# Kernel optimization log

Measured on AMD Instinct MI355X. Metric: run time of the kernel, lower is better.

The kernel has to match this reference:

```python
import math
import jax, jax.numpy as jnp
import numpy as np

GRAIN = 300   # bilinear / grain dim (gpconv output channels)
PAD = 4       # explicit zero padding before each conv1d / conv2d
POOL = 40     # adaptive pool target (mf_model_pool_dim)

def conv1d_k2(x, w, b):
    # x: [B, L, Cin], w: [Cout, Cin, 2] -> [B, L-1, Cout]
    return (jnp.einsum('blc,oc->blo', x[:, :-1], w[:, :, 0])
            + jnp.einsum('blc,oc->blo', x[:, 1:], w[:, :, 1]) + b)

def kmax_last(x, k):
    # torch-style k-max pooling: top-k values along last axis, original order kept
    idx = jnp.sort(jax.lax.top_k(x, k)[1], axis=-1)
    return jnp.take_along_axis(x, idx, axis=-1)

def kmax_len(x, k):
    # k-max pooling over the length axis (axis=1) of [B, L, C]
    return jnp.swapaxes(kmax_last(jnp.swapaxes(x, 1, 2), k), 1, 2)

def adaptive_max_1d(x, out, axis):
    # torch AdaptiveMaxPool semantics along one axis; windows precomputed statically
    L = x.shape[axis]
    r = np.arange(out)
    starts = (r * L) // out
    ends = -((-(r + 1) * L) // out)
    maxw = int((ends - starts).max())
    off = starts[:, None] + np.arange(maxw)[None, :]
    mask = jnp.asarray(off < ends[:, None])
    idxs = np.minimum(off, L - 1)
    xm = jnp.moveaxis(x, axis, -1)
    g = jnp.where(mask, xm[..., idxs], -jnp.inf)
    return jnp.moveaxis(g.max(-1), -1, axis)

def conv2d_p4(x, w, b):
    y = jax.lax.conv_general_dilated(x, w, (1, 1), [(PAD, PAD), (PAD, PAD)],
                                     dimension_numbers=('NCHW', 'OIHW', 'NCHW'))
    return y + b[None, :, None, None]

def gp_tower(x, w1, b1, w2, b2, w3, b3, k1, k2):
    # multigranular conv tower: zero-pad(4) -> conv1d(k=2) -> tanh -> k-max pool
    g0 = kmax_last(x, GRAIN)                      # [B, L, 300]
    def block(z, w, b, k):
        z = jnp.pad(z, ((0, 0), (PAD, PAD), (0, 0)))
        return kmax_len(jnp.tanh(conv1d_k2(z, w, b)), k)
    p1 = block(x, w1, b1, k1)                     # [B, k1, 300]
    p2 = block(p1, w2, b2, k2)                    # [B, k2, 300]
    p3 = block(p2, w3, b3, 1)                     # [B, 1, 300]
    return jnp.concatenate([g0, p1, p2, p3], axis=1)

def _forward(query, pos_doc, neg_docs, qw1, qb1, qw2, qb2, qw3, qb3,
             dw1, db1, dw2, db2, dw3, db3, bw, bb,
             mw1, mb1, mw2, mb2, mw3, mb3, lw, lb):
    B, Lq, _ = query.shape
    S, _, Ld, _ = neg_docs.shape
    kq1, kq2 = max(4, math.ceil(2 * Lq / 3)), max(4, math.ceil(Lq / 3))
    kd1, kd2 = max(4, math.ceil(2 * Ld / 3)), max(4, math.ceil(Ld / 3))
    qg = gp_tower(query, qw1, qb1, qw2, qb2, qw3, qb3, kq1, kq2)   # [B, Nq, 300]
    docs = jnp.concatenate([pos_doc[None], neg_docs], 0).reshape((S + 1) * B, Ld, -1)
    dg = gp_tower(docs, dw1, db1, dw2, db2, dw3, db3, kd1, kd2)    # [(S+1)B, Nd, 300]
    Nq, Nd = qg.shape[1], dg.shape[1]
    dg = dg.reshape(S + 1, B, Nd, GRAIN)
    # batched bilinear matching + sigmoid (replaces the O(Nq*Nd) per-pair loop)
    qt = jnp.einsum('bqd,de->bqe', qg, bw)
    M = jax.nn.sigmoid(jnp.einsum('bqe,sbje->sbqj', qt, dg) + bb[0])
    M = M.reshape((S + 1) * B, Nq, Nd)
    x = adaptive_max_1d(adaptive_max_1d(M, POOL, 1), POOL, 2)[:, None]  # [N,1,40,40]
    for w, b in ((mw1, mb1), (mw2, mb2), (mw3, mb3)):
        x = jax.nn.sigmoid(conv2d_p4(x, w, b))
        x = adaptive_max_1d(adaptive_max_1d(x, POOL, 2), POOL, 3)
        x = x.max(axis=1, keepdims=True)          # k-max(k=1) over channels
    feat = x[:, 0]                                # [N, 40, 40]
    h = jax.nn.sigmoid(jnp.einsum('nij,j->ni', feat, lw[0]) + lb[0])
    s = jax.nn.sigmoid(h @ lw[0] + lb[0])
    return s.reshape(S + 1, B)                    # row 0 = pos-doc scores

def setup_inputs():
    ks = jax.random.split(jax.random.key(0), 26)
    def n(i, shape, s=0.05):
        return jax.random.normal(ks[i], shape, dtype=jnp.float32) * s
    return dict(
        query=jax.random.normal(ks[0], (16, 239, 1024), dtype=jnp.float32),
        pos_doc=jax.random.normal(ks[1], (16, 479, 1024), dtype=jnp.float32),
        neg_docs=jax.random.normal(ks[2], (4, 16, 479, 1024), dtype=jnp.float32),
        qw1=n(3, (300, 1024, 2)), qb1=n(4, (300,)),
        qw2=n(5, (300, 300, 2)), qb2=n(6, (300,)),
        qw3=n(7, (300, 300, 2)), qb3=n(8, (300,)),
        dw1=n(9, (300, 1024, 2)), db1=n(10, (300,)),
        dw2=n(11, (300, 300, 2)), db2=n(12, (300,)),
        dw3=n(13, (300, 300, 2)), db3=n(14, (300,)),
        bw=n(15, (300, 300)), bb=n(16, (1,)),
        mw1=n(17, (50, 1, 2, 2)), mb1=n(18, (50,)),
        mw2=n(19, (50, 1, 2, 2)), mb2=n(20, (50,)),
        mw3=n(21, (50, 1, 2, 2)), mb3=n(22, (50,)),
        lw=n(23, (1, 40)), lb=n(24, (1,)),
    )

def reference(query, pos_doc, neg_docs, qw1, qb1, qw2, qb2, qw3, qb3,
              dw1, db1, dw2, db2, dw3, db3, bw, bb,
              mw1, mb1, mw2, mb2, mw3, mb3, lw, lb):
    return _forward(query, pos_doc, neg_docs, qw1, qb1, qw2, qb2, qw3, qb3,
                    dw1, db1, dw2, db2, dw3, db3, bw, bb,
                    mw1, mb1, mw2, mb2, mw3, mb3, lw, lb)
```

## Files before the change

kernel.cpp:

```cpp
#include <hip/hip_runtime.h>
#include <hip/hip_bf16.h>
#include <math.h>

typedef unsigned long long ull;
typedef unsigned int uint;
typedef unsigned short ushort_t;

typedef short bf16x8 __attribute__((ext_vector_type(8)));
typedef float floatx4 __attribute__((ext_vector_type(4)));

__device__ inline ushort_t f2b(float f) {
    uint u = __float_as_uint(f);
    u = u + 0x7fffu + ((u >> 16) & 1u);
    return (ushort_t)(u >> 16);
}

__device__ inline uint kmap16(ushort_t u) {
    return (u & 0x8000u) ? (uint)((~u) & 0xFFFFu) : (uint)(u | 0x8000u);
}
__device__ inline ushort_t kinv16(uint k) {
    return (k & 0x8000u) ? (ushort_t)(k ^ 0x8000u) : (ushort_t)((~k) & 0xFFFFu);
}

__device__ inline void async_copy16(const void* g, void* l) {
    __builtin_amdgcn_global_load_lds(
        (const __attribute__((address_space(1))) void*)g,
        (__attribute__((address_space(3))) void*)l, 16, 0, 0);
}

__global__ void prep_w2_kernel(const float* __restrict__ w, ushort_t* __restrict__ Wb,
                               int C, int CP) {
    int CHn = CP / 32;
    int total = CHn * 2 * 20 * 512;
    for (int i = blockIdx.x * blockDim.x + threadIdx.x; i < total;
         i += gridDim.x * blockDim.x) {
        int e = i & 7;
        int lane = (i >> 3) & 63;
        int rest = i >> 9;
        int g = rest % 20;
        int tc = rest / 20;
        int t = tc & 1, c = tc >> 1;
        int o = g * 16 + (lane & 15);
        int ch = c * 32 + (lane >> 4) * 8 + e;
        float v = (o < 300 && ch < C) ? w[((size_t)o * C + ch) * 2 + t] : 0.f;
        Wb[i] = f2b(v);
    }
}

__global__ void prep_bw_kernel(const float* __restrict__ bw, ushort_t* __restrict__ bwb) {
    int i = blockIdx.x * 256 + threadIdx.x;
    if (i >= 320 * 320) return;
    int e = i / 320, d = i - e * 320;
    bwb[i] = (e < 300 && d < 300) ? f2b(bw[d * 300 + e]) : (ushort_t)0;
}

__global__ __launch_bounds__(256) void x_pad_bf16_kernel(
    const float* __restrict__ src, const float* __restrict__ src2, int split_n,
    long long s_nstr, int Lin, ushort_t* __restrict__ dst, int rows)
{
    int r = blockIdx.x, n = blockIdx.y;
    const float* sp = (split_n > 0 && n >= split_n)
                          ? src2 + (size_t)(n - split_n) * s_nstr
                          : src + (size_t)n * s_nstr;
    int g = r - 4;
    ushort_t* dp = dst + ((size_t)n * rows + r) * 1024;
    int c = threadIdx.x * 4;
    ushort4 o = {0, 0, 0, 0};
    if (g >= 0 && g < Lin) {
        float4 v = *(const float4*)&sp[(size_t)g * 1024 + c];
        o.x = f2b(v.x); o.y = f2b(v.y); o.z = f2b(v.z); o.w = f2b(v.w);
    }
    *(ushort4*)&dp[c] = o;
}

template <int CP>
__global__ __launch_bounds__(256, 3) void conv_wave_kernel(
    const ushort_t* __restrict__ xq, long long xq_nstr,
    const ushort_t* __restrict__ xd, long long xd_nstr,
    const ushort_t* __restrict__ Wq, const ushort_t* __restrict__ Wd,
    const float* __restrict__ bq, const float* __restrict__ bd,
    int Lout_q, int Lout_d, int mtiles_q, int mtiles_d,
    ushort_t* __restrict__ yt)
{
    constexpr int CH = CP / 32;
    __shared__ char Abuf[4][3][4160];

    int tid = threadIdx.x, wid = tid >> 6, lane = tid & 63;
    int u = blockIdx.x * 4 + wid;
    int md5 = mtiles_d * 5, DOCU = md5 * 80;

    const ushort_t* x; const ushort_t* W; const float* bias;
    int Lout, mt, nt, ng;
    if (u < DOCU) {
        int nd = u / md5, r = u - nd * md5;
        mt = r / 5; nt = r - mt * 5;
        x = xd + (size_t)nd * xd_nstr; W = Wd; bias = bd; Lout = Lout_d;
        ng = 16 + nd;
    } else {
        int v = u - DOCU, mq5 = mtiles_q * 5;
        int nq = v / mq5, r = v - nq * mq5;
        mt = r / 5; nt = r - mt * 5;
        x = xq + (size_t)nq * xq_nstr; W = Wq; bias = bq; Lout = Lout_q;
        ng = nq;
    }
    int l0 = mt * 64;
    int lrow = lane & 15, quad = lane >> 4;

    const ushort_t* gMain = x + (size_t)(l0 + (lane >> 2)) * CP
                              + ((lane & 3) ^ ((lane >> 3) & 3)) * 8;
    const ushort_t* gXtra = x + (size_t)(l0 + 64) * CP + lane * 8;

    const ushort_t* Bw = W + (size_t)(nt * 4) * 512 + lane * 8;

    int offA[2][4];
#pragma unroll
    for (int t = 0; t < 2; t++)
#pragma unroll
        for (int ms = 0; ms < 4; ms++) {
            int r = ms * 16 + lrow + t;
            offA[t][ms] = r * 64 + ((quad ^ ((r >> 1) & 3)) << 4);
        }

    floatx4 acc[4][4];
#pragma unroll
    for (int i = 0; i < 4; i++)
#pragma unroll
        for (int j = 0; j < 4; j++) acc[i][j] = (floatx4){0.f, 0.f, 0.f, 0.f};

    char* lb0 = &Abuf[wid][0][0];

    auto STAGE = [&](int cc, int slot) {
        char* lb = lb0 + slot * 4160;
        const ushort_t* gs = gMain + cc * 32;
        async_copy16(gs, lb);
        async_copy16(gs + (size_t)16 * CP, lb + 1024);
        async_copy16(gs + (size_t)32 * CP, lb + 2048);
        async_copy16(gs + (size_t)48 * CP, lb + 3072);
        if (lane < 4) async_copy16(gXtra + cc * 32, lb + 4096);
    };

    STAGE(0, 0);
    STAGE(1, 1);

    for (int c = 0; c < CH; c++) {
        if (c == 0) asm volatile("s_waitcnt vmcnt(5)" ::: "memory");
        else        asm volatile("s_waitcnt vmcnt(8)" ::: "memory");
        __builtin_amdgcn_sched_barrier(0);

        bf16x8 bf[2][4];
#pragma unroll
        for (int t = 0; t < 2; t++)
#pragma unroll
            for (int ns = 0; ns < 4; ns++)
                bf[t][ns] = *(const bf16x8*)(Bw + (size_t)((c * 2 + t) * 20 + ns) * 512);
        __builtin_amdgcn_sched_barrier(0x38F);

        if (c + 2 < CH) STAGE(c + 2, (c + 2) % 3);

        const char* ab = lb0 + (c % 3) * 4160;
        __builtin_amdgcn_s_setprio(1);
#pragma unroll
        for (int t = 0; t < 2; t++) {
            bf16x8 af[4];
#pragma unroll
            for (int ms = 0; ms < 4; ms++)
                af[ms] = *(const bf16x8*)(ab + offA[t][ms]);
#pragma unroll
            for (int ms = 0; ms < 4; ms++)
#pragma unroll
                for (int ns = 0; ns < 4; ns++)
                    acc[ms][ns] = __builtin_amdgcn_mfma_f32_16x16x32_bf16(
                        af[ms], bf[t][ns], acc[ms][ns], 0, 0, 0);
        }
        __builtin_amdgcn_s_setprio(0);
    }

    ushort_t* yp = yt + (size_t)ng * (320 * 488);
#pragma unroll
    for (int ns = 0; ns < 4; ns++) {
        int o = nt * 64 + ns * 16 + lrow;
        if (o >= 300) continue;
        float bo = bias[o];
        ushort_t* orow = yp + (size_t)o * 488;
#pragma unroll
        for (int ms = 0; ms < 4; ms++) {
            int l = l0 + ms * 16 + quad * 4;
            if (l + 3 < Lout) {
                ushort4 v;
                v.x = f2b(tanhf(acc[ms][ns][0] + bo));
                v.y = f2b(tanhf(acc[ms][ns][1] + bo));
                v.z = f2b(tanhf(acc[ms][ns][2] + bo));
                v.w = f2b(tanhf(acc[ms][ns][3] + bo));
                *(ushort4*)&orow[l] = v;
            } else {
#pragma unroll
                for (int r = 0; r < 4; r++)
                    if (l + r < Lout) orow[l + r] = f2b(tanhf(acc[ms][ns][r] + bo));
            }
        }
    }
}

__global__ __launch_bounds__(256) void topk_g0_kernel(
    const ushort_t* __restrict__ src, int CC, long long s_n,
    ushort_t* __restrict__ out, long long o_n, long long o_c)
{
    __shared__ uint hist[4][257];

    int tid = threadIdx.x, wid = tid >> 6, lane = tid & 63;
    int row = blockIdx.x * 4 + wid;
    int n = row / CC, c = row - n * CC;
    const ushort_t* sp = src + (size_t)n * s_n + (size_t)c * 1024;

    const uint* sp32 = (const uint*)(sp + (size_t)lane * 16);
    uint pk[8];
    {
        uint4 va = *(const uint4*)sp32;
        uint4 vb = *(const uint4*)(sp32 + 4);
        pk[0] = va.x; pk[1] = va.y; pk[2] = va.z; pk[3] = va.w;
        pk[4] = vb.x; pk[5] = vb.y; pk[6] = vb.z; pk[7] = vb.w;
    }
    uint key[16];
#pragma unroll
    for (int i = 0; i < 8; i++) {
        uint w = pk[i];
        uint s = w & 0x80008000u;
        w ^= 0x80008000u | ((s >> 15) * 0x7fffu);
        key[2 * i] = w & 0xffffu;
        key[2 * i + 1] = w >> 16;
    }

    uint* hg = hist[wid];
    uint rem = 300, bsel = 0, T = 0;

#pragma unroll
    for (int round = 0; round < 2; round++) {
#pragma unroll
        for (int t = 0; t < 4; t++) hg[lane + t * 64] = 0;
        __builtin_amdgcn_sched_barrier(0);
        if (round == 0) {
#pragma unroll
            for (int e = 0; e < 16; e++) atomicAdd(&hg[key[e] >> 8], 1u);
        } else {
#pragma unroll
            for (int e = 0; e < 16; e++)
                if ((key[e] >> 8) == bsel) atomicAdd(&hg[key[e] & 255u], 1u);
        }
        __builtin_amdgcn_sched_barrier(0);
        uint hv[4], Sr = 0;
#pragma unroll
        for (int t = 0; t < 4; t++) { hv[t] = hg[lane * 4 + t]; Sr += hv[t]; }
        uint suf = Sr;
#pragma unroll
        for (int off = 1; off < 64; off <<= 1) {
            uint u = __shfl_down(suf, off);
            if (lane + off < 64) suf += u;
        }
        uint acc = suf - Sr;
        uint found = 0;
#pragma unroll
        for (int t = 3; t >= 0; t--) {
            uint h = hv[t];
            if (!found && acc < rem && acc + h >= rem)
                found = ((uint)(lane * 4 + t) << 16) | (rem - acc);
            acc += h;
        }
#pragma unroll
        for (int off = 1; off < 64; off <<= 1) found |= __shfl_xor(found, off);
        if (round == 0) {
            bsel = found >> 16;
            rem = found & 0xffffu;
        } else {
            T = (bsel << 8) | (found >> 16);
            rem = found & 0xffffu;
        }
        __builtin_amdgcn_sched_barrier(0);
    }

    uint gtc = 0, eqc = 0;
#pragma unroll
    for (int e = 0; e < 16; e++) {
        gtc += (key[e] > T) ? 1u : 0u;
        eqc += (key[e] == T) ? 1u : 0u;
    }
    uint pack = (gtc << 16) | eqc, incl = pack;
#pragma unroll
    for (int off = 1; off < 64; off <<= 1) {
        uint u = __shfl_up(incl, off);
        if (lane >= off) incl += u;
    }
    uint excl = incl - pack;
    uint gt_b = excl >> 16, eq_b = excl & 0xffffu;

    ushort_t* dp = out + (size_t)n * o_n + (size_t)c * o_c;
#pragma unroll
    for (int e = 0; e < 16; e++) {
        uint kk = key[e];
        if (kk > T) {
            uint pos = gt_b + (eq_b < rem ? eq_b : rem);
            dp[pos] = kinv16(kk);
            gt_b++;
        } else if (kk == T) {
            if (eq_b < rem) dp[gt_b + eq_b] = kinv16(kk);
            eq_b++;
        }
    }
}

__global__ __launch_bounds__(256) void topk_cols_kernel(
    const ushort_t* __restrict__ yt2,
    int Lq, int Ld, int kq, int kd,
    ushort_t* __restrict__ qg, int qoff,
    ushort_t* __restrict__ dg, int doff,
    ushort_t* __restrict__ pq, long long pq_nstr,
    ushort_t* __restrict__ pd, long long pd_nstr)
{
    __shared__ __align__(16) ushort_t xin[32][488];
    __shared__ __align__(16) uint hist[32 * 257];
    ushort_t* otile = (ushort_t*)hist;

    int cg = blockIdx.x, n = blockIdx.y;
    int c0 = cg * 32;
    bool isq = (n < 16);
    int L = isq ? Lq : Ld;
    int k = isq ? kq : kd;
    int nd = isq ? n : n - 16;
    int tid = threadIdx.x;

    const ushort_t* src = yt2 + (size_t)n * (320 * 488) + (size_t)c0 * 488;
    for (int i = tid; i < 32 * 61; i += 256) {
        int j = i / 61, s = i - j * 61;
        *(uint4*)&xin[j][s * 8] = *(const uint4*)&src[(size_t)j * 488 + s * 8];
    }
    __syncthreads();

    int g = tid >> 3, r = tid & 7;
    uint* hg = &hist[g * 257];
    bool cval = (c0 + g) < 300;
    int S = (L + 7) >> 3;
    int llo = r * S, lhi = llo + S;
    if (lhi > L) lhi = L;
    if (llo > L) llo = L;

    uint rem = (uint)k;
    uint bsel = 0;
    uint Tt = 0;

#pragma unroll
    for (int round = 0; round < 2; round++) {
        for (int t = r; t < 256; t += 8) hg[t] = 0;
        for (int l = llo; l < lhi; l++) {
            uint key = cval ? kmap16(xin[g][l]) : 0x8000u;
            if (round == 0)
                atomicAdd(&hg[key >> 8], 1u);
            else if ((key >> 8) == bsel)
                atomicAdd(&hg[key & 255u], 1u);
        }
        uint hv[32];
        uint Sr = 0;
        int b0 = r * 32;
#pragma unroll
        for (int t = 0; t < 32; t++) { hv[t] = hg[b0 + t]; Sr += hv[t]; }
        uint suf = Sr;
#pragma unroll
        for (int off = 1; off < 8; off <<= 1) {
            uint u = __shfl_down(suf, off);
            if (r + off < 8) suf += u;
        }
        uint acc = suf - Sr;
        uint found = 0;
#pragma unroll
        for (int t = 31; t >= 0; t--) {
            uint h = hv[t];
            if (!found && acc < rem && acc + h >= rem)
                found = ((uint)(b0 + t) << 16) | (rem - acc);
            acc += h;
        }
#pragma unroll
        for (int off = 1; off < 8; off <<= 1) found |= __shfl_xor(found, off);
        if (round == 0) {
            bsel = found >> 16;
            rem = found & 0xffffu;
        } else {
            Tt = (bsel << 8) | (found >> 16);
            rem = found & 0xffffu;
        }
    }

    uint gtc = 0, eqc = 0;
    for (int l = llo; l < lhi; l++) {
        uint key = cval ? kmap16(xin[g][l]) : 0x8000u;
        gtc += (key > Tt) ? 1u : 0u;
        eqc += (key == Tt) ? 1u : 0u;
    }
    uint pack = (gtc << 16) | eqc, incl = pack;
#pragma unroll
    for (int off = 1; off < 8; off <<= 1) {
        uint u = __shfl_up(incl, off);
        if (r >= off) incl += u;
    }
    uint excl = incl - pack;
    uint gt_b = excl >> 16, eq_b = excl & 0xffffu;

    __syncthreads();

    for (int l = llo; l < lhi; l++) {
        uint key = cval ? kmap16(xin[g][l]) : 0x8000u;
        if (key > Tt) {
            uint pos = gt_b + (eq_b < rem ? eq_b : rem);
            otile[pos * 32 + g] = kinv16(key);
            gt_b++;
        } else if (key == Tt) {
            if (eq_b < rem) otile[(gt_b + eq_b) * 32 + g] = kinv16(key);
            eq_b++;
        }
    }
    __syncthreads();

    ushort_t* d1 = isq ? qg + ((size_t)nd * 480 + qoff) * 320 + c0
                       : dg + ((size_t)nd * 960 + doff) * 320 + c0;
    ushort_t* d2 = 0;
    if (isq) { if (pq) d2 = pq + (size_t)nd * pq_nstr + 4 * 320 + c0; }
    else     { if (pd) d2 = pd + (size_t)nd * pd_nstr + 4 * 320 + c0; }

    for (int i = tid; i < k * 8; i += 256) {
        int p = i >> 3, s = i & 7;
        ushort4 v = *(ushort4*)&otile[p * 32 + s * 4];
        *(ushort4*)&d1[(size_t)p * 320 + s * 4] = v;
        if (d2) *(ushort4*)&d2[(size_t)p * 320 + s * 4] = v;
    }
}

__global__ __launch_bounds__(256) void qt_mfma_kernel(
    const ushort_t* __restrict__ qgb, const ushort_t* __restrict__ bwb,
    ushort_t* __restrict__ qtb)
{
    int mt = blockIdx.x, b = blockIdx.y;
    int tid = threadIdx.x, wid = tid >> 6, lane = tid & 63;
    int wn = wid * 80, lrow = lane & 15, quad = lane >> 4;

    const ushort_t* A = qgb + ((size_t)b * 480 + mt * 48 + lrow) * 320 + quad * 8;
    const ushort_t* B = bwb + (size_t)(wn + lrow) * 320 + quad * 8;

    floatx4 acc[3][5];
#pragma unroll
    for (int i = 0; i < 3; i++)
#pragma unroll
        for (int j = 0; j < 5; j++) acc[i][j] = (floatx4){0.f, 0.f, 0.f, 0.f};

#pragma unroll 5
    for (int c0 = 0; c0 < 320; c0 += 32) {
        bf16x8 af[3], bfr[5];
#pragma unroll
        for (int ms = 0; ms < 3; ms++)
            af[ms] = *(const bf16x8*)&A[(size_t)(ms * 16) * 320 + c0];
#pragma unroll
        for (int ns = 0; ns < 5; ns++)
            bfr[ns] = *(const bf16x8*)&B[(size_t)(ns * 16) * 320 + c0];
#pragma unroll
        for (int ms = 0; ms < 3; ms++)
#pragma unroll
            for (int ns = 0; ns < 5; ns++)
                acc[ms][ns] = __builtin_amdgcn_mfma_f32_16x16x32_bf16(
                    af[ms], bfr[ns], acc[ms][ns], 0, 0, 0);
    }

    ushort_t* out = qtb + ((size_t)b * 480 + mt * 48) * 320;
#pragma unroll
    for (int ms = 0; ms < 3; ms++)
#pragma unroll
        for (int ns = 0; ns < 5; ns++)
#pragma unroll
            for (int r = 0; r < 4; r++)
                out[(size_t)(ms * 16 + quad * 4 + r) * 320 + wn + ns * 16 + lrow] =
                    f2b(acc[ms][ns][r]);
}

__global__ __launch_bounds__(256) void mpool_mfma_kernel(
    const ushort_t* __restrict__ qtb16, const ushort_t* __restrict__ dgb16,
    const float* __restrict__ bb, float* __restrict__ mp)
{
    __shared__ float pool[2 * 12 * 192];

    int jb = blockIdx.x;
    int qb = blockIdx.y;
    int n  = blockIdx.z;
    int b  = n & 15;

    int tid = threadIdx.x;
    int wid = tid >> 6, lane = tid & 63;
    int wm2 = wid >> 1;
    int wm = wm2 * 48, wn = (wid & 1) * 96;
    int lrow = lane & 15, quad = lane >> 4;

    const ushort_t* Abase = qtb16 + ((size_t)b * 480 + qb * 96 + wm) * 320 + quad * 8;
    const ushort_t* Bbase = dgb16 + ((size_t)n * 960 + jb * 192 + wn) * 320 + quad * 8;

    floatx4 acc[3][6];
#pragma unroll
    for (int i = 0; i < 3; i++)
#pragma unroll
        for (int j = 0; j < 6; j++) acc[i][j] = (floatx4){0.f, 0.f, 0.f, 0.f};

#pragma unroll 2
    for (int c0 = 0; c0 < 320; c0 += 32) {
        bf16x8 af[3], bfr[6];
#pragma unroll
        for (int mt = 0; mt < 3; mt++)
            af[mt] = *(const bf16x8*)&Abase[(size_t)(mt * 16 + lrow) * 320 + c0];
#pragma unroll
        for (int nt = 0; nt < 6; nt++)
            bfr[nt] = *(const bf16x8*)&Bbase[(size_t)(nt * 16 + lrow) * 320 + c0];
#pragma unroll
        for (int mt = 0; mt < 3; mt++)
#pragma unroll
            for (int nt = 0; nt < 6; nt++)
                acc[mt][nt] = __builtin_amdgcn_mfma_f32_16x16x32_bf16(
                    af[mt], bfr[nt], acc[mt][nt], 0, 0, 0);
    }

#pragma unroll
    for (int mt = 0; mt < 3; mt++) {
        int g = mt * 4 + quad;
#pragma unroll
        for (int nt = 0; nt < 6; nt++) {
            floatx4 a = acc[mt][nt];
            float rm = fmaxf(fmaxf(a[0], a[1]), fmaxf(a[2], a[3]));
            pool[(wm2 * 12 + g) * 192 + wn + nt * 16 + lrow] = rm;
        }
    }
    __syncthreads();

    if (tid < 64) {
        int qw = tid >> 3, jw = tid & 7;
        int slab = qw >> 2, w = qw & 3;
        float m = -INFINITY;
        const float* pp = &pool[(slab * 12 + w * 3) * 192 + jw * 24];
        for (int g = 0; g < 3; g++)
            for (int cc = 0; cc < 24; cc++)
                m = fmaxf(m, pp[g * 192 + cc]);
        float sig = 1.f / (1.f + expf(-(m + bb[0])));
        mp[(size_t)n * 1600 + (size_t)(qb * 8 + qw) * 40 + (jb * 8 + jw)] = sig;
    }
}

#define OCG 10
__global__ __launch_bounds__(256) void convblock_atomic_kernel(
    const float* __restrict__ X, const float* __restrict__ w,
    const float* __restrict__ bias, uint* __restrict__ Y)
{
    __shared__ float xp[48 * 48];
    __shared__ float ys[47 * 47];
    __shared__ float t1[40 * 47];
    __shared__ float outacc[1600];

    int n = blockIdx.x, t = threadIdx.x;
    int oc0 = blockIdx.y * OCG;
    const float* xn = X + (size_t)n * 1600;
    for (int i = t; i < 48 * 48; i += 256) {
        int r = i / 48, c = i - r * 48;
        int rr = r - 4, cc = c - 4;
        xp[i] = (rr >= 0 && rr < 40 && cc >= 0 && cc < 40) ? xn[rr * 40 + cc] : 0.f;
    }
    for (int i = t; i < 1600; i += 256) outacc[i] = 0.f;
    __syncthreads();

    for (int oc = oc0; oc < oc0 + OCG; oc++) {
        float w00 = w[oc * 4 + 0], w01 = w[oc * 4 + 1];
        float w10 = w[oc * 4 + 2], w11 = w[oc * 4 + 3];
        float bo = bias[oc];
        for (int i = t; i < 47 * 47; i += 256) {
            int r = i / 47, c = i - r * 47;
            float v = xp[r * 48 + c] * w00 + xp[r * 48 + c + 1] * w01
                    + xp[(r + 1) * 48 + c] * w10 + xp[(r + 1) * 48 + c + 1] * w11 + bo;
            ys[i] = 1.f / (1.f + expf(-v));
        }
        __syncthreads();
        for (int i = t; i < 40 * 47; i += 256) {
            int r = i / 47, c = i - r * 47;
            int s = (47 * r) / 40, e = (47 * (r + 1) + 39) / 40;
            float m = ys[s * 47 + c];
            for (int x = s + 1; x < e; x++) m = fmaxf(m, ys[x * 47 + c]);
            t1[i] = m;
        }
        __syncthreads();
        for (int i = t; i < 1600; i += 256) {
            int r = i / 40, c = i - r * 40;
            int s = (47 * c) / 40, e = (47 * (c + 1) + 39) / 40;
            float m = t1[r * 47 + s];
            for (int x = s + 1; x < e; x++) m = fmaxf(m, t1[r * 47 + x]);
            outacc[i] = fmaxf(outacc[i], m);
        }
        __syncthreads();
    }
    for (int i = t; i < 1600; i += 256)
        atomicMax(&Y[(size_t)n * 1600 + i], __float_as_uint(outacc[i]));
}

__global__ __launch_bounds__(64) void head_kernel(
    const float* __restrict__ feat, const float* __restrict__ lw,
    const float* __restrict__ lb, float* __restrict__ out)
{
    __shared__ float hs[40];
    int n = blockIdx.x, t = threadIdx.x;
    const float* f = feat + (size_t)n * 1600;
    if (t < 40) {
        float a = 0.f;
        for (int j = 0; j < 40; j++) a += f[t * 40 + j] * lw[j];
        hs[t] = 1.f / (1.f + expf(-(a + lb[0])));
    }
    __syncthreads();
    if (t == 0) {
        float a = 0.f;
        for (int i = 0; i < 40; i++) a += hs[i] * lw[i];
        out[n] = 1.f / (1.f + expf(-(a + lb[0])));
    }
}

extern "C" void kernel_launch(void* const* d_in, const int* in_sizes, int n_in,
                              void* d_out, int out_size, void* d_ws, size_t ws_size,
                              hipStream_t stream) {
    const float* query    = (const float*)d_in[0];
    const float* pos_doc  = (const float*)d_in[1];
    const float* neg_docs = (const float*)d_in[2];
    const float* qw1 = (const float*)d_in[3];  const float* qb1 = (const float*)d_in[4];
    const float* qw2 = (const float*)d_in[5];  const float* qb2 = (const float*)d_in[6];
    const float* qw3 = (const float*)d_in[7];  const float* qb3 = (const float*)d_in[8];
    const float* dw1 = (const float*)d_in[9];  const float* db1 = (const float*)d_in[10];
    const float* dw2 = (const float*)d_in[11]; const float* db2 = (const float*)d_in[12];
    const float* dw3 = (const float*)d_in[13]; const float* db3 = (const float*)d_in[14];
    const float* bw  = (const float*)d_in[15]; const float* bb  = (const float*)d_in[16];
    const float* mw1 = (const float*)d_in[17]; const float* mb1 = (const float*)d_in[18];
    const float* mw2 = (const float*)d_in[19]; const float* mb2 = (const float*)d_in[20];
    const float* mw3 = (const float*)d_in[21]; const float* mb3 = (const float*)d_in[22];
    const float* lw  = (const float*)d_in[23]; const float* lb  = (const float*)d_in[24];

    float* ws = (float*)d_ws;
    ushort_t* qw1b  = (ushort_t*)(ws + 0);
    ushort_t* qw2b  = (ushort_t*)(ws + 327680);
    ushort_t* qw3b  = (ushort_t*)(ws + 430080);
    ushort_t* dw1b  = (ushort_t*)(ws + 532480);
    ushort_t* dw2b  = (ushort_t*)(ws + 860160);
    ushort_t* dw3b  = (ushort_t*)(ws + 962560);
    ushort_t* bwb   = (ushort_t*)(ws + 1064960);
    ushort_t* qgb16 = (ushort_t*)(ws + 1116160);
    ushort_t* dgb16 = (ushort_t*)(ws + 2344960);
    ushort_t* yt    = (ushort_t*)(ws + 14632960);
    ushort_t* qxb   = (ushort_t*)(ws + 22128640);
    ushort_t* p1q   = (ushort_t*)(ws + 22128640);
    ushort_t* p2q   = (ushort_t*)(ws + 22640640);
    ushort_t* dxb   = (ushort_t*)(ws + 24291328);
    ushort_t* p1d   = (ushort_t*)(ws + 24291328);
    ushort_t* p2d   = (ushort_t*)(ws + 28899328);
    ushort_t* qtb16 = (ushort_t*)(ws + 31459328);
    float*    mp    = ws + 32688128;
    float*    ya    = ws + 32816128;
    float*    yb    = ws + 32944128;
    float*    yc    = ws + 33072128;

    prep_w2_kernel<<<1280, 256, 0, stream>>>(qw1, qw1b, 1024, 1024);
    prep_w2_kernel<<<400, 256, 0, stream>>>(qw2, qw2b, 300, 320);
    prep_w2_kernel<<<400, 256, 0, stream>>>(qw3, qw3b, 300, 320);
    prep_w2_kernel<<<1280, 256, 0, stream>>>(dw1, dw1b, 1024, 1024);
    prep_w2_kernel<<<400, 256, 0, stream>>>(dw2, dw2b, 300, 320);
    prep_w2_kernel<<<400, 256, 0, stream>>>(dw3, dw3b, 300, 320);
    prep_bw_kernel<<<400, 256, 0, stream>>>(bw, bwb);

    {
        dim3 g(264, 16);
        x_pad_bf16_kernel<<<g, 256, 0, stream>>>(query, nullptr, 0,
                                                 239LL * 1024, 239, qxb, 264);
    }
    {
        dim3 g(520, 80);
        x_pad_bf16_kernel<<<g, 256, 0, stream>>>(pos_doc, neg_docs, 16,
                                                 479LL * 1024, 479, dxb, 520);
    }

    topk_g0_kernel<<<(16 * 239) / 4, 256, 0, stream>>>(
        qxb + 4 * 1024, 239, 264LL * 1024, qgb16, 480LL * 320, 320);
    topk_g0_kernel<<<(80 * 479) / 4, 256, 0, stream>>>(
        dxb + 4 * 1024, 479, 520LL * 1024, dgb16, 960LL * 320, 320);

    conv_wave_kernel<1024><<<880, 256, 0, stream>>>(
        qxb, 264LL * 1024, dxb, 520LL * 1024,
        qw1b, dw1b, qb1, db1, 246, 486, 4, 8, yt);

    hipMemsetAsync(p1q, 0, 16 * 200 * 320 * 2, stream);
    hipMemsetAsync(p2q, 0, 16 * 104 * 320 * 2, stream);
    hipMemsetAsync(p1d, 0, (size_t)80 * 360 * 320 * 2, stream);
    hipMemsetAsync(p2d, 0, (size_t)80 * 200 * 320 * 2, stream);
    hipMemsetAsync(ya, 0, 80 * 1600 * 4, stream);
    hipMemsetAsync(yb, 0, 80 * 1600 * 4, stream);
    hipMemsetAsync(yc, 0, 80 * 1600 * 4, stream);

    {
        dim3 g(10, 96);
        topk_cols_kernel<<<g, 256, 0, stream>>>(
            yt, 246, 486, 160, 320,
            qgb16, 239, dgb16, 479,
            p1q, 200LL * 320, p1d, 360LL * 320);
    }

    conv_wave_kernel<320><<<660, 256, 0, stream>>>(
        p1q, 200LL * 320, p1d, 360LL * 320,
        qw2b, dw2b, qb2, db2, 167, 327, 3, 6, yt);

    {
        dim3 g(10, 96);
        topk_cols_kernel<<<g, 256, 0, stream>>>(
            yt, 167, 327, 80, 160,
            qgb16, 399, dgb16, 799,
            p2q, 104LL * 320, p2d, 200LL * 320);
    }

    conv_wave_kernel<320><<<340, 256, 0, stream>>>(
        p2q, 104LL * 320, p2d, 200LL * 320,
        qw3b, dw3b, qb3, db3, 87, 167, 2, 3, yt);

    {
        dim3 g(10, 96);
        topk_cols_kernel<<<g, 256, 0, stream>>>(
            yt, 87, 167, 1, 1,
            qgb16, 479, dgb16, 959,
            nullptr, 0, nullptr, 0);
    }

    {
        dim3 g(10, 16);
        qt_mfma_kernel<<<g, 256, 0, stream>>>(qgb16, bwb, qtb16);
    }
    {
        dim3 g(5, 5, 80);
        mpool_mfma_kernel<<<g, 256, 0, stream>>>(qtb16, dgb16, bb, mp);
    }

    {
        dim3 g(80, 5);
        convblock_atomic_kernel<<<g, 256, 0, stream>>>(mp, mw1, mb1, (uint*)ya);
        convblock_atomic_kernel<<<g, 256, 0, stream>>>(ya, mw2, mb2, (uint*)yb);
        convblock_atomic_kernel<<<g, 256, 0, stream>>>(yb, mw3, mb3, (uint*)yc);
    }
    head_kernel<<<80, 64, 0, stream>>>(yc, lw, lb, (float*)d_out);
}
```

Before: 1.074 ms.

## Enlarge conv wave M-tile to 128 rows with register double-buffered weights

Each wave in the conv1d MFMA kernel now computes 128 output positions instead of 64. This doubles reuse of each loaded weight fragment and halves the number of waves and blocks launched. The A staging moves from triple to double buffering in LDS, and the B fragments are prefetched into alternating register sets so weight loads overlap compute. In exchange the accumulator register footprint doubles, the occupancy hint drops from 3 to 2, and the larger tiles read rows past the valid length of the padded layer-2/3 buffers.

```diff
diff --git a/kernel.cpp b/kernel.cpp
--- a/kernel.cpp
+++ b/kernel.cpp
@@ -74,7 +74,7 @@
 }
 
 template <int CP>
-__global__ __launch_bounds__(256, 3) void conv_wave_kernel(
+__global__ __launch_bounds__(256, 2) void conv_wave_kernel(
     const ushort_t* __restrict__ xq, long long xq_nstr,
     const ushort_t* __restrict__ xd, long long xd_nstr,
     const ushort_t* __restrict__ Wq, const ushort_t* __restrict__ Wd,
@@ -83,7 +83,8 @@
     ushort_t* __restrict__ yt)
 {
     constexpr int CH = CP / 32;
-    __shared__ char Abuf[4][3][4160];
+    constexpr int SLOT = 129 * 64;
+    __shared__ char Abuf[4][2][SLOT];
 
     int tid = threadIdx.x, wid = tid >> 6, lane = tid & 63;
     int u = blockIdx.x * 4 + wid;
@@ -103,76 +104,94 @@
         x = xq + (size_t)nq * xq_nstr; W = Wq; bias = bq; Lout = Lout_q;
         ng = nq;
     }
-    int l0 = mt * 64;
+    int l0 = mt * 128;
     int lrow = lane & 15, quad = lane >> 4;
 
     const ushort_t* gMain = x + (size_t)(l0 + (lane >> 2)) * CP
                               + ((lane & 3) ^ ((lane >> 3) & 3)) * 8;
-    const ushort_t* gXtra = x + (size_t)(l0 + 64) * CP + lane * 8;
+    const ushort_t* gXtra = x + (size_t)(l0 + 128) * CP + lane * 8;
 
     const ushort_t* Bw = W + (size_t)(nt * 4) * 512 + lane * 8;
 
-    int offA[2][4];
+    int offA[2][8];
 #pragma unroll
     for (int t = 0; t < 2; t++)
 #pragma unroll
-        for (int ms = 0; ms < 4; ms++) {
+        for (int ms = 0; ms < 8; ms++) {
             int r = ms * 16 + lrow + t;
             offA[t][ms] = r * 64 + ((quad ^ ((r >> 1) & 3)) << 4);
         }
 
-    floatx4 acc[4][4];
-#pragma unroll
-    for (int i = 0; i < 4; i++)
+    floatx4 acc[8][4];
+#pragma unroll
+    for (int i = 0; i < 8; i++)
 #pragma unroll
         for (int j = 0; j < 4; j++) acc[i][j] = (floatx4){0.f, 0.f, 0.f, 0.f};
 
     char* lb0 = &Abuf[wid][0][0];
 
     auto STAGE = [&](int cc, int slot) {
-        char* lb = lb0 + slot * 4160;
+        char* lb = lb0 + slot * SLOT;
         const ushort_t* gs = gMain + cc * 32;
-        async_copy16(gs, lb);
-        async_copy16(gs + (size_t)16 * CP, lb + 1024);
-        async_copy16(gs + (size_t)32 * CP, lb + 2048);
-        async_copy16(gs + (size_t)48 * CP, lb + 3072);
-        if (lane < 4) async_copy16(gXtra + cc * 32, lb + 4096);
+#pragma unroll
+        for (int g = 0; g < 8; g++)
+            async_copy16(gs + (size_t)(g * 16) * CP, lb + g * 1024);
+        if (lane < 4) async_copy16(gXtra + cc * 32, lb + 8192);
     };
-
-    STAGE(0, 0);
-    STAGE(1, 1);
-
-    for (int c = 0; c < CH; c++) {
-        if (c == 0) asm volatile("s_waitcnt vmcnt(5)" ::: "memory");
-        else        asm volatile("s_waitcnt vmcnt(8)" ::: "memory");
-        __builtin_amdgcn_sched_barrier(0);
-
-        bf16x8 bf[2][4];
+    auto LOADB = [&](bf16x8 (&bf)[2][4], int cc) {
 #pragma unroll
         for (int t = 0; t < 2; t++)
 #pragma unroll
             for (int ns = 0; ns < 4; ns++)
-                bf[t][ns] = *(const bf16x8*)(Bw + (size_t)((c * 2 + t) * 20 + ns) * 512);
-        __builtin_amdgcn_sched_barrier(0x38F);
-
-        if (c + 2 < CH) STAGE(c + 2, (c + 2) % 3);
-
-        const char* ab = lb0 + (c % 3) * 4160;
+                bf[t][ns] = *(const bf16x8*)(Bw + (size_t)((cc * 2 + t) * 20 + ns) * 512);
+    };
+    auto COMPUTE = [&](bf16x8 (&bf)[2][4], int slot) {
+        const char* ab = lb0 + slot * SLOT;
         __builtin_amdgcn_s_setprio(1);
 #pragma unroll
         for (int t = 0; t < 2; t++) {
-            bf16x8 af[4];
-#pragma unroll
-            for (int ms = 0; ms < 4; ms++)
+            bf16x8 af[8];
+#pragma unroll
+            for (int ms = 0; ms < 8; ms++)
                 af[ms] = *(const bf16x8*)(ab + offA[t][ms]);
 #pragma unroll
-            for (int ms = 0; ms < 4; ms++)
+            for (int ms = 0; ms < 8; ms++)
 #pragma unroll
                 for (int ns = 0; ns < 4; ns++)
                     acc[ms][ns] = __builtin_amdgcn_mfma_f32_16x16x32_bf16(
                         af[ms], bf[t][ns], acc[ms][ns], 0, 0, 0);
         }
         __builtin_amdgcn_s_setprio(0);
+    };
+    auto WAITA = [&]() {
+        asm volatile("s_waitcnt vmcnt(8)" ::: "memory");
+        __builtin_amdgcn_sched_barrier(0);
+    };
+
+    bf16x8 bA[2][4], bB[2][4];
+
+    STAGE(0, 0);
+    __builtin_amdgcn_sched_barrier(0x38F);
+    LOADB(bA, 0);
+
+    for (int c = 0; c < CH; c += 2) {
+        WAITA();
+        if (c + 1 < CH) {
+            STAGE(c + 1, (c + 1) & 1);
+            __builtin_amdgcn_sched_barrier(0x38F);
+            LOADB(bB, c + 1);
+            __builtin_amdgcn_sched_barrier(0x38F);
+        }
+        COMPUTE(bA, c & 1);
+
+        WAITA();
+        if (c + 2 < CH) {
+            STAGE(c + 2, (c + 2) & 1);
+            __builtin_amdgcn_sched_barrier(0x38F);
+            LOADB(bA, c + 2);
+            __builtin_amdgcn_sched_barrier(0x38F);
+        }
+        COMPUTE(bB, (c + 1) & 1);
     }
 
     ushort_t* yp = yt + (size_t)ng * (320 * 488);
@@ -183,7 +202,7 @@
         float bo = bias[o];
         ushort_t* orow = yp + (size_t)o * 488;
 #pragma unroll
-        for (int ms = 0; ms < 4; ms++) {
+        for (int ms = 0; ms < 8; ms++) {
             int l = l0 + ms * 16 + quad * 4;
             if (l + 3 < Lout) {
                 ushort4 v;
@@ -682,9 +701,9 @@
     topk_g0_kernel<<<(80 * 479) / 4, 256, 0, stream>>>(
         dxb + 4 * 1024, 479, 520LL * 1024, dgb16, 960LL * 320, 320);
 
-    conv_wave_kernel<1024><<<880, 256, 0, stream>>>(
+    conv_wave_kernel<1024><<<440, 256, 0, stream>>>(
         qxb, 264LL * 1024, dxb, 520LL * 1024,
-        qw1b, dw1b, qb1, db1, 246, 486, 4, 8, yt);
+        qw1b, dw1b, qb1, db1, 246, 486, 2, 4, yt);
 
     hipMemsetAsync(p1q, 0, 16 * 200 * 320 * 2, stream);
     hipMemsetAsync(p2q, 0, 16 * 104 * 320 * 2, stream);
@@ -702,9 +721,9 @@
             p1q, 200LL * 320, p1d, 360LL * 320);
     }
 
-    conv_wave_kernel<320><<<660, 256, 0, stream>>>(
+    conv_wave_kernel<320><<<340, 256, 0, stream>>>(
         p1q, 200LL * 320, p1d, 360LL * 320,
-        qw2b, dw2b, qb2, db2, 167, 327, 3, 6, yt);
+        qw2b, dw2b, qb2, db2, 167, 327, 2, 3, yt);
 
     {
         dim3 g(10, 96);
@@ -714,9 +733,9 @@
             p2q, 104LL * 320, p2d, 200LL * 320);
     }
 
-    conv_wave_kernel<320><<<340, 256, 0, stream>>>(
+    conv_wave_kernel<320><<<220, 256, 0, stream>>>(
         p2q, 104LL * 320, p2d, 200LL * 320,
-        qw3b, dw3b, qb3, db3, 87, 167, 2, 3, yt);
+        qw3b, dw3b, qb3, db3, 87, 167, 1, 2, yt);
 
     {
         dim3 g(10, 96);
```

New measurement: 1.237 ms. +15.2%, slower.
